# Kernel tuning notes

Hardware: AMD Instinct MI355X
Metric: run time of the kernel (lower is better)

## Reference

```python
import jax, jax.numpy as jnp
import numpy as np

C1 = 256
C2 = 256
C = 256

def setup_inputs() -> dict:
    key = jax.random.key(0)
    ks = jax.random.split(key, 8)
    B, S, H, W = 4, 8, 32, 32
    img_feat = jax.random.normal(ks[0], (B, S, C1, H, W), dtype=jnp.float32)
    depth_feat = jax.random.normal(ks[1], (B, S, C2, H, W), dtype=jnp.float32)
    sq = 1.0 / np.sqrt(C1)
    sk = 1.0 / np.sqrt(C2)
    Wq = jax.random.uniform(ks[2], (C1, C), jnp.float32, -sq, sq)
    bq = jax.random.uniform(ks[3], (C,), jnp.float32, -sq, sq)
    Wk = jax.random.uniform(ks[4], (C2, C), jnp.float32, -sk, sk)
    bk = jax.random.uniform(ks[5], (C,), jnp.float32, -sk, sk)
    Wv = jax.random.uniform(ks[6], (C2, C), jnp.float32, -sk, sk)
    bv = jax.random.uniform(ks[7], (C,), jnp.float32, -sk, sk)
    return {"img_feat": img_feat, "depth_feat": depth_feat,
            "Wq": Wq, "bq": bq, "Wk": Wk, "bk": bk, "Wv": Wv, "bv": bv}

def reference(img_feat, depth_feat, Wq, bq, Wk, bk, Wv, bv):
    B, S, _, H, W = img_feat.shape
    hw = H * W
    # channels-last, flatten spatial: [B,S,hw,c1]
    img = jnp.transpose(img_feat, (0, 1, 3, 4, 2)).reshape(B, S, hw, -1)
    depth = jnp.transpose(depth_feat, (0, 1, 3, 4, 2)).reshape(B, S, hw, -1)
    q = (img @ Wq + bq).astype(jnp.float32)    # [B,S,hw,c]
    k = (depth @ Wk + bk).astype(jnp.float32)  # [B,S,hw,c]
    v = (depth @ Wv + bv).astype(jnp.float32)  # [B,S,hw,c]
    scale = 1.0 / jnp.sqrt(jnp.float32(Wq.shape[1]))
    scores = jnp.einsum('bsqc,bskc->bsqk', q, k) * scale  # [B,S,hw,hw]
    attn = jax.nn.softmax(scores, axis=-1)
    out = jnp.einsum('bsqk,bskc->bsqc', attn, v)          # [B,S,hw,c]
    out = out + img                                        # residual (c == c1)
    out = out.reshape(B, S, H, W, -1).astype(img_feat.dtype)
    return jnp.transpose(out, (0, 1, 4, 2, 3))             # [B,S,c,H,W]
```

## Files before the change

### kernel.cpp

```cpp
#include <hip/hip_runtime.h>
#include <hip/hip_bf16.h>

typedef __hip_bfloat16 bf16;
typedef __attribute__((ext_vector_type(8))) short short8v;
typedef __attribute__((ext_vector_type(4))) float f32x4;

#define NSLICE 32
#define HW     1024
#define CDIM   256
#define KVT    32

__global__ __launch_bounds__(256)
void wt_prep_kernel(const float* __restrict__ Wq, const float* __restrict__ Wk,
                    const float* __restrict__ Wv, bf16* __restrict__ wt)
{
    const int m = blockIdx.x >> 8;
    const int r = blockIdx.x & 255;
    const int tid = threadIdx.x;
    const float* W = (m == 0) ? Wq : (m == 1) ? Wk : Wv;
    const float sc = (m == 0) ? 0.0625f : 1.0f;
    wt[((size_t)m << 16) + (size_t)tid * 256 + r] = __float2bfloat16(W[r * 256 + tid] * sc);
}

__global__ __launch_bounds__(256)
void proj_q_kernel(const float* __restrict__ img, const bf16* __restrict__ wt,
                   const float* __restrict__ bq, bf16* __restrict__ qo)
{
    const int bid   = blockIdx.x;
    const int s     = (bid & 7) * 4 + ((bid >> 3) & 3);
    const int tt    = (bid >> 5) & 15;
    const int chalf = bid >> 9;
    const int t0    = tt * 64;

    const int tid  = threadIdx.x;
    const int wave = tid >> 6;
    const int lane = tid & 63;
    const int lo16 = lane & 15;
    const int hi4  = lane >> 4;
    const int cw0  = chalf * 128 + wave * 32;

    __shared__ short Ai[64][40];

    const int so = tid >> 6, st = tid & 63;
    const float* imgS = img + (size_t)s * CDIM * HW + t0;

    f32x4 aq[2][4];
    #pragma unroll
    for (int a = 0; a < 2; ++a)
        #pragma unroll
        for (int b = 0; b < 4; ++b) aq[a][b] = (f32x4){0.f, 0.f, 0.f, 0.f};

    float ri[8];
    #pragma unroll
    for (int j = 0; j < 8; ++j) ri[j] = imgS[(size_t)(so * 8 + j) * HW + st];

    for (int kc = 0; kc < 8; ++kc) {
        __syncthreads();
        {
            short ti[8];
            #pragma unroll
            for (int j = 0; j < 8; ++j) {
                bf16 hb = __float2bfloat16(ri[j]);
                ti[j] = *reinterpret_cast<short*>(&hb);
            }
            *reinterpret_cast<short8v*>(&Ai[st][so * 8]) = *reinterpret_cast<short8v*>(ti);
        }
        __syncthreads();

        if (kc < 7) {
            #pragma unroll
            for (int j = 0; j < 8; ++j)
                ri[j] = imgS[(size_t)((kc + 1) * 32 + so * 8 + j) * HW + st];
        }

        short8v xi[4];
        #pragma unroll
        for (int nf = 0; nf < 4; ++nf)
            xi[nf] = *reinterpret_cast<const short8v*>(&Ai[nf * 16 + lo16][hi4 * 8]);

        const int koff = kc * 32 + hi4 * 8;
        short8v wqf[2];
        #pragma unroll
        for (int mf = 0; mf < 2; ++mf)
            wqf[mf] = *reinterpret_cast<const short8v*>(
                wt + (size_t)(cw0 + mf * 16 + lo16) * 256 + koff);

        #pragma unroll
        for (int mf = 0; mf < 2; ++mf)
            #pragma unroll
            for (int nf = 0; nf < 4; ++nf)
                aq[mf][nf] = __builtin_amdgcn_mfma_f32_16x16x32_bf16(wqf[mf], xi[nf], aq[mf][nf], 0, 0, 0);
    }

    #pragma unroll
    for (int mf = 0; mf < 2; ++mf) {
        const int cb = cw0 + mf * 16 + 4 * hi4;
        const float4 b4 = *reinterpret_cast<const float4*>(bq + cb);
        const float ba[4] = {b4.x * 0.0625f, b4.y * 0.0625f, b4.z * 0.0625f, b4.w * 0.0625f};
        #pragma unroll
        for (int nf = 0; nf < 4; ++nf) {
            const int tok = t0 + nf * 16 + lo16;
            bf16 tq[4];
            #pragma unroll
            for (int g = 0; g < 4; ++g)
                tq[g] = __float2bfloat16(aq[mf][nf][g] + ba[g]);
            *reinterpret_cast<uint2*>(&qo[((size_t)s * HW + tok) * CDIM + cb]) =
                *reinterpret_cast<uint2*>(tq);
        }
    }
}

__global__ __launch_bounds__(256)
void proj_kv_kernel(const float* __restrict__ dep, const bf16* __restrict__ wt,
                    const float* __restrict__ bk, const float* __restrict__ bv,
                    bf16* __restrict__ ko, bf16* __restrict__ vt)
{
    const int bid   = blockIdx.x;
    const int s     = (bid & 7) * 4 + ((bid >> 3) & 3);
    const int tt    = (bid >> 5) & 15;
    const int chalf = bid >> 9;
    const int t0    = tt * 64;

    const int tid  = threadIdx.x;
    const int wave = tid >> 6;
    const int lane = tid & 63;
    const int lo16 = lane & 15;
    const int hi4  = lane >> 4;
    const int cw0  = chalf * 128 + wave * 32;

    __shared__ short Ad[64][40];

    const int so = tid >> 6, st = tid & 63;
    const float* depS = dep + (size_t)s * CDIM * HW + t0;
    const bf16* wtk = wt + (1 << 16);
    const bf16* wtv = wt + (2 << 16);

    f32x4 ak[2][4], av[4][2];
    #pragma unroll
    for (int a = 0; a < 2; ++a)
        #pragma unroll
        for (int b = 0; b < 4; ++b) {
            ak[a][b] = (f32x4){0.f, 0.f, 0.f, 0.f};
            av[b][a] = (f32x4){0.f, 0.f, 0.f, 0.f};
        }

    float rd[8];
    #pragma unroll
    for (int j = 0; j < 8; ++j) rd[j] = depS[(size_t)(so * 8 + j) * HW + st];

    for (int kc = 0; kc < 8; ++kc) {
        __syncthreads();
        {
            short td[8];
            #pragma unroll
            for (int j = 0; j < 8; ++j) {
                bf16 hb = __float2bfloat16(rd[j]);
                td[j] = *reinterpret_cast<short*>(&hb);
            }
            *reinterpret_cast<short8v*>(&Ad[st][so * 8]) = *reinterpret_cast<short8v*>(td);
        }
        __syncthreads();

        if (kc < 7) {
            #pragma unroll
            for (int j = 0; j < 8; ++j)
                rd[j] = depS[(size_t)((kc + 1) * 32 + so * 8 + j) * HW + st];
        }

        short8v xd[4];
        #pragma unroll
        for (int nf = 0; nf < 4; ++nf)
            xd[nf] = *reinterpret_cast<const short8v*>(&Ad[nf * 16 + lo16][hi4 * 8]);

        const int koff = kc * 32 + hi4 * 8;
        short8v wkf[2], wvf[2];
        #pragma unroll
        for (int mf = 0; mf < 2; ++mf) {
            const size_t wrow = (size_t)(cw0 + mf * 16 + lo16) * 256 + koff;
            wkf[mf] = *reinterpret_cast<const short8v*>(wtk + wrow);
            wvf[mf] = *reinterpret_cast<const short8v*>(wtv + wrow);
        }

        #pragma unroll
        for (int mf = 0; mf < 2; ++mf)
            #pragma unroll
            for (int nf = 0; nf < 4; ++nf)
                ak[mf][nf] = __builtin_amdgcn_mfma_f32_16x16x32_bf16(wkf[mf], xd[nf], ak[mf][nf], 0, 0, 0);
        #pragma unroll
        for (int mf = 0; mf < 4; ++mf)
            #pragma unroll
            for (int nf = 0; nf < 2; ++nf)
                av[mf][nf] = __builtin_amdgcn_mfma_f32_16x16x32_bf16(xd[mf], wvf[nf], av[mf][nf], 0, 0, 0);
    }

    #pragma unroll
    for (int mf = 0; mf < 2; ++mf) {
        const int cb = cw0 + mf * 16 + 4 * hi4;
        const float4 b4 = *reinterpret_cast<const float4*>(bk + cb);
        const float ba[4] = {b4.x, b4.y, b4.z, b4.w};
        #pragma unroll
        for (int nf = 0; nf < 4; ++nf) {
            const int tok = t0 + nf * 16 + lo16;
            bf16 tk[4];
            #pragma unroll
            for (int g = 0; g < 4; ++g)
                tk[g] = __float2bfloat16(ak[mf][nf][g] + ba[g]);
            *reinterpret_cast<uint2*>(&ko[((size_t)s * HW + tok) * CDIM + cb]) =
                *reinterpret_cast<uint2*>(tk);
        }
    }
    #pragma unroll
    for (int nf = 0; nf < 2; ++nf) {
        const int c = cw0 + nf * 16 + lo16;
        const float bvv = bv[c];
        #pragma unroll
        for (int mf = 0; mf < 4; ++mf) {
            const int tb = t0 + mf * 16 + 4 * hi4;
            bf16 tv[4];
            #pragma unroll
            for (int g = 0; g < 4; ++g)
                tv[g] = __float2bfloat16(av[mf][nf][g] + bvv);
            *reinterpret_cast<uint2*>(&vt[((size_t)s * CDIM + c) * HW + tb]) =
                *reinterpret_cast<uint2*>(tv);
        }
    }
}

__global__ __launch_bounds__(256)
void flash_mfma_kernel(const bf16* __restrict__ q, const bf16* __restrict__ k,
                       const bf16* __restrict__ vt, const float* __restrict__ img,
                       float* __restrict__ out)
{
    const int bid = blockIdx.x;
    const int s   = (bid & 7) * 4 + ((bid >> 3) & 3);
    const int t0  = (bid >> 5) * 64;

    const int tid  = threadIdx.x;
    const int wave = tid >> 6;
    const int lane = tid & 63;
    const int lo16 = lane & 15;
    const int hi4  = lane >> 4;

    __shared__ short KsL[32 * 256];
    __shared__ short VsL[256 * 32];
    __shared__ short PsL[4 * 16 * 32];

    short8v qf[8];
    {
        const bf16* qp = q + ((size_t)s * HW + t0 + wave * 16 + lo16) * CDIM + hi4 * 8;
        #pragma unroll
        for (int kf = 0; kf < 8; ++kf)
            qf[kf] = *reinterpret_cast<const short8v*>(qp + kf * 32);
    }

    f32x4 Oacc[16];
    #pragma unroll
    for (int cf = 0; cf < 16; ++cf) Oacc[cf] = (f32x4){0.f, 0.f, 0.f, 0.f};
    float lp[4] = {0.f, 0.f, 0.f, 0.f};

    const bf16* kS  = k  + (size_t)s * HW * CDIM;
    const bf16* vtS = vt + (size_t)s * CDIM * HW;

    const int krow = tid >> 3;
    const int kch  = tid & 7;
    const int kxor = krow & 7;
    const int vxor = (tid >> 1) & 3;

    short8v kreg[4], vreg[4];
    #pragma unroll
    for (int u = 0; u < 4; ++u) {
        kreg[u] = *reinterpret_cast<const short8v*>(kS + (size_t)krow * CDIM + (kch + 8 * u) * 8);
        vreg[u] = *reinterpret_cast<const short8v*>(vtS + (size_t)tid * HW + u * 8);
    }

    const int pvRow = lo16 * 32 + (hi4 ^ ((lo16 >> 1) & 3)) * 8;
    for (int kt = 0; kt < HW / KVT; ++kt) {
        __syncthreads();
        #pragma unroll
        for (int u = 0; u < 4; ++u)
            *reinterpret_cast<short8v*>(&KsL[krow * 256 + ((kch ^ kxor) + 8 * u) * 8]) = kreg[u];
        #pragma unroll
        for (int u = 0; u < 4; ++u)
            *reinterpret_cast<short8v*>(&VsL[tid * 32 + (u ^ vxor) * 8]) = vreg[u];
        __syncthreads();

        if (kt + 1 < HW / KVT) {
            const bf16* src = kS + (size_t)(kt + 1) * KVT * CDIM;
            #pragma unroll
            for (int u = 0; u < 4; ++u) {
                kreg[u] = *reinterpret_cast<const short8v*>(src + (size_t)krow * CDIM + (kch + 8 * u) * 8);
                vreg[u] = *reinterpret_cast<const short8v*>(vtS + (size_t)tid * HW + (kt + 1) * KVT + u * 8);
            }
        }

        f32x4 sa[2];
        sa[0] = (f32x4){0.f, 0.f, 0.f, 0.f};
        sa[1] = (f32x4){0.f, 0.f, 0.f, 0.f};
        __builtin_amdgcn_s_setprio(1);
        #pragma unroll
        for (int ks = 0; ks < 8; ++ks) {
            #pragma unroll
            for (int cf = 0; cf < 2; ++cf) {
                const int row = cf * 16 + lo16;
                short8v bfr = *reinterpret_cast<const short8v*>(
                    &KsL[row * 256 + ((4 * ks + hi4) ^ (lo16 & 7)) * 8]);
                sa[cf] = __builtin_amdgcn_mfma_f32_16x16x32_bf16(qf[ks], bfr, sa[cf], 0, 0, 0);
            }
        }
        __builtin_amdgcn_s_setprio(0);

        #pragma unroll
        for (int cf = 0; cf < 2; ++cf)
            #pragma unroll
            for (int g = 0; g < 4; ++g) {
                const float e = __expf(sa[cf][g]);
                lp[g] += e;
                bf16 hb = __float2bfloat16(e);
                const int r = 4 * hi4 + g;
                const int ch = (2 * cf + (lo16 >> 3)) ^ ((r >> 1) & 3);
                PsL[wave * 512 + r * 32 + ch * 8 + (lo16 & 7)] = *reinterpret_cast<short*>(&hb);
            }

        const short8v pa = *reinterpret_cast<const short8v*>(&PsL[wave * 512 + pvRow]);

        __builtin_amdgcn_s_setprio(1);
        #pragma unroll
        for (int cf = 0; cf < 16; ++cf) {
            const int row = cf * 16 + lo16;
            const short8v vb = *reinterpret_cast<const short8v*>(
                &VsL[row * 32 + (hi4 ^ ((lo16 >> 1) & 3)) * 8]);
            Oacc[cf] = __builtin_amdgcn_mfma_f32_16x16x32_bf16(pa, vb, Oacc[cf], 0, 0, 0);
        }
        __builtin_amdgcn_s_setprio(0);
    }

    float inv[4];
    #pragma unroll
    for (int g = 0; g < 4; ++g) {
        float l = lp[g];
        #pragma unroll
        for (int off = 1; off < 16; off <<= 1) l += __shfl_xor(l, off);
        inv[g] = 1.0f / l;
    }
    const float* imgS = img + (size_t)s * CDIM * HW;
    float*       outS = out + (size_t)s * CDIM * HW;
    const int tt = t0 + wave * 16 + 4 * hi4;
    #pragma unroll
    for (int cf = 0; cf < 16; ++cf) {
        const int c = cf * 16 + lo16;
        const float4 r4 = *reinterpret_cast<const float4*>(imgS + (size_t)c * HW + tt);
        float4 o;
        o.x = Oacc[cf][0] * inv[0] + r4.x;
        o.y = Oacc[cf][1] * inv[1] + r4.y;
        o.z = Oacc[cf][2] * inv[2] + r4.z;
        o.w = Oacc[cf][3] * inv[3] + r4.w;
        *reinterpret_cast<float4*>(outS + (size_t)c * HW + tt) = o;
    }
}

extern "C" void kernel_launch(void* const* d_in, const int* in_sizes, int n_in,
                              void* d_out, int out_size, void* d_ws, size_t ws_size,
                              hipStream_t stream)
{
    const float* img = (const float*)d_in[0];
    const float* dep = (const float*)d_in[1];
    const float* Wq  = (const float*)d_in[2];
    const float* bq  = (const float*)d_in[3];
    const float* Wk  = (const float*)d_in[4];
    const float* bk  = (const float*)d_in[5];
    const float* Wv  = (const float*)d_in[6];
    const float* bv  = (const float*)d_in[7];
    float* out = (float*)d_out;

    const size_t npt  = (size_t)NSLICE * HW * CDIM;
    const size_t need = 3 * npt * sizeof(bf16) + 3 * 65536 * sizeof(bf16);
    if (ws_size < need) {
        hipMemsetAsync(d_out, 0, (size_t)out_size * sizeof(float), stream);
        return;
    }

    bf16* q  = (bf16*)d_ws;
    bf16* k  = q + npt;
    bf16* vt = k + npt;
    bf16* wt = vt + npt;

    wt_prep_kernel<<<dim3(3 * 256), 256, 0, stream>>>(Wq, Wk, Wv, wt);

    proj_q_kernel<<<dim3(NSLICE * 32), 256, 0, stream>>>(img, wt, bq, q);
    proj_kv_kernel<<<dim3(NSLICE * 32), 256, 0, stream>>>(dep, wt, bk, bv, k, vt);

    flash_mfma_kernel<<<dim3(NSLICE * 16), 256, 0, stream>>>(q, k, vt, img, out);
}
```

Baseline: 123.0 us.

## Double KV tile to 64, compute S transposed, and pass P via shuffles

The flash attention kernel now stages 64-key K and V^T tiles per iteration instead of 32, halving the number of barrier-synchronized iterations. QK^T is computed as K·Q so each lane holds probabilities along keys, and the P operand for the PV MFMA is built with cross-lane shuffles rather than a round trip through LDS. Row sums are reduced differently to match the transposed layout, and launch bounds request two blocks per SM. The cost is doubled LDS (64KB), more registers for prefetch buffers, and many shuffles, which may limit occupancy.

```diff
diff --git a/kernel.cpp b/kernel.cpp
--- a/kernel.cpp
+++ b/kernel.cpp
@@ -4,11 +4,11 @@
 typedef __hip_bfloat16 bf16;
 typedef __attribute__((ext_vector_type(8))) short short8v;
 typedef __attribute__((ext_vector_type(4))) float f32x4;
+typedef __attribute__((ext_vector_type(4))) unsigned int u32x4;
 
 #define NSLICE 32
 #define HW     1024
 #define CDIM   256
-#define KVT    32
 
 __global__ __launch_bounds__(256)
 void wt_prep_kernel(const float* __restrict__ Wq, const float* __restrict__ Wk,
@@ -226,7 +226,7 @@
     }
 }
 
-__global__ __launch_bounds__(256)
+__global__ __launch_bounds__(256, 2)
 void flash_mfma_kernel(const bf16* __restrict__ q, const bf16* __restrict__ k,
                        const bf16* __restrict__ vt, const float* __restrict__ img,
                        float* __restrict__ out)
@@ -241,9 +241,8 @@
     const int lo16 = lane & 15;
     const int hi4  = lane >> 4;
 
-    __shared__ short KsL[32 * 256];
-    __shared__ short VsL[256 * 32];
-    __shared__ short PsL[4 * 16 * 32];
+    __shared__ short KsL[64 * 256];
+    __shared__ short VsL[256 * 64];
 
     short8v qf[8];
     {
@@ -256,92 +255,114 @@
     f32x4 Oacc[16];
     #pragma unroll
     for (int cf = 0; cf < 16; ++cf) Oacc[cf] = (f32x4){0.f, 0.f, 0.f, 0.f};
-    float lp[4] = {0.f, 0.f, 0.f, 0.f};
+    float lp = 0.f;
 
     const bf16* kS  = k  + (size_t)s * HW * CDIM;
     const bf16* vtS = vt + (size_t)s * CDIM * HW;
 
-    const int krow = tid >> 3;
-    const int kch  = tid & 7;
-    const int kxor = krow & 7;
-    const int vxor = (tid >> 1) & 3;
-
-    short8v kreg[4], vreg[4];
-    #pragma unroll
-    for (int u = 0; u < 4; ++u) {
-        kreg[u] = *reinterpret_cast<const short8v*>(kS + (size_t)krow * CDIM + (kch + 8 * u) * 8);
+    const int krow = tid >> 2;
+    const int kseg = tid & 3;
+    const int kx   = krow & 7;
+    const int vx   = tid & 7;
+
+    short8v kreg[8], vreg[8];
+    #pragma unroll
+    for (int u = 0; u < 8; ++u) {
+        kreg[u] = *reinterpret_cast<const short8v*>(kS + (size_t)krow * CDIM + kseg * 64 + u * 8);
         vreg[u] = *reinterpret_cast<const short8v*>(vtS + (size_t)tid * HW + u * 8);
     }
 
-    const int pvRow = lo16 * 32 + (hi4 ^ ((lo16 >> 1) & 3)) * 8;
-    for (int kt = 0; kt < HW / KVT; ++kt) {
-        __syncthreads();
-        #pragma unroll
-        for (int u = 0; u < 4; ++u)
-            *reinterpret_cast<short8v*>(&KsL[krow * 256 + ((kch ^ kxor) + 8 * u) * 8]) = kreg[u];
-        #pragma unroll
-        for (int u = 0; u < 4; ++u)
-            *reinterpret_cast<short8v*>(&VsL[tid * 32 + (u ^ vxor) * 8]) = vreg[u];
-        __syncthreads();
-
-        if (kt + 1 < HW / KVT) {
-            const bf16* src = kS + (size_t)(kt + 1) * KVT * CDIM;
-            #pragma unroll
-            for (int u = 0; u < 4; ++u) {
-                kreg[u] = *reinterpret_cast<const short8v*>(src + (size_t)krow * CDIM + (kch + 8 * u) * 8);
-                vreg[u] = *reinterpret_cast<const short8v*>(vtS + (size_t)tid * HW + (kt + 1) * KVT + u * 8);
+    const int src0 = lo16 + 16 * (2 * (hi4 & 1));
+    const int src1 = src0 + 16;
+    const bool sel = hi4 >= 2;
+
+    for (int kt = 0; kt < 16; ++kt) {
+        __syncthreads();
+        #pragma unroll
+        for (int u = 0; u < 8; ++u)
+            *reinterpret_cast<short8v*>(&KsL[krow * 256 + ((kseg * 8 + u) ^ kx) * 8]) = kreg[u];
+        #pragma unroll
+        for (int u = 0; u < 8; ++u)
+            *reinterpret_cast<short8v*>(&VsL[tid * 64 + (u ^ vx) * 8]) = vreg[u];
+        __syncthreads();
+
+        if (kt + 1 < 16) {
+            const bf16* ksrc = kS + (size_t)(kt + 1) * 64 * CDIM;
+            #pragma unroll
+            for (int u = 0; u < 8; ++u) {
+                kreg[u] = *reinterpret_cast<const short8v*>(ksrc + (size_t)krow * CDIM + kseg * 64 + u * 8);
+                vreg[u] = *reinterpret_cast<const short8v*>(vtS + (size_t)tid * HW + (kt + 1) * 64 + u * 8);
             }
         }
 
-        f32x4 sa[2];
-        sa[0] = (f32x4){0.f, 0.f, 0.f, 0.f};
-        sa[1] = (f32x4){0.f, 0.f, 0.f, 0.f};
+        f32x4 sa[4];
+        #pragma unroll
+        for (int m = 0; m < 4; ++m) sa[m] = (f32x4){0.f, 0.f, 0.f, 0.f};
         __builtin_amdgcn_s_setprio(1);
         #pragma unroll
         for (int ks = 0; ks < 8; ++ks) {
             #pragma unroll
-            for (int cf = 0; cf < 2; ++cf) {
-                const int row = cf * 16 + lo16;
-                short8v bfr = *reinterpret_cast<const short8v*>(
-                    &KsL[row * 256 + ((4 * ks + hi4) ^ (lo16 & 7)) * 8]);
-                sa[cf] = __builtin_amdgcn_mfma_f32_16x16x32_bf16(qf[ks], bfr, sa[cf], 0, 0, 0);
+            for (int m = 0; m < 4; ++m) {
+                const short8v kfr = *reinterpret_cast<const short8v*>(
+                    &KsL[(16 * m + lo16) * 256 + ((4 * ks + hi4) ^ (lo16 & 7)) * 8]);
+                sa[m] = __builtin_amdgcn_mfma_f32_16x16x32_bf16(kfr, qf[ks], sa[m], 0, 0, 0);
             }
         }
         __builtin_amdgcn_s_setprio(0);
 
-        #pragma unroll
-        for (int cf = 0; cf < 2; ++cf)
-            #pragma unroll
-            for (int g = 0; g < 4; ++g) {
-                const float e = __expf(sa[cf][g]);
-                lp[g] += e;
-                bf16 hb = __float2bfloat16(e);
-                const int r = 4 * hi4 + g;
-                const int ch = (2 * cf + (lo16 >> 3)) ^ ((r >> 1) & 3);
-                PsL[wave * 512 + r * 32 + ch * 8 + (lo16 & 7)] = *reinterpret_cast<short*>(&hb);
+        unsigned int pk[4][2];
+        #pragma unroll
+        for (int m = 0; m < 4; ++m) {
+            float e0 = __expf(sa[m][0]), e1 = __expf(sa[m][1]);
+            float e2 = __expf(sa[m][2]), e3 = __expf(sa[m][3]);
+            lp += (e0 + e1) + (e2 + e3);
+            bf16 h0 = __float2bfloat16(e0), h1 = __float2bfloat16(e1);
+            bf16 h2 = __float2bfloat16(e2), h3 = __float2bfloat16(e3);
+            pk[m][0] = (unsigned int)*reinterpret_cast<unsigned short*>(&h0) |
+                       ((unsigned int)*reinterpret_cast<unsigned short*>(&h1) << 16);
+            pk[m][1] = (unsigned int)*reinterpret_cast<unsigned short*>(&h2) |
+                       ((unsigned int)*reinterpret_cast<unsigned short*>(&h3) << 16);
+        }
+
+        short8v pfr[2];
+        #pragma unroll
+        for (int c = 0; c < 2; ++c) {
+            const unsigned int a0 = (unsigned int)__shfl((int)pk[2 * c][0], src0);
+            const unsigned int b0 = (unsigned int)__shfl((int)pk[2 * c + 1][0], src0);
+            const unsigned int a1 = (unsigned int)__shfl((int)pk[2 * c][1], src0);
+            const unsigned int b1 = (unsigned int)__shfl((int)pk[2 * c + 1][1], src0);
+            const unsigned int a2 = (unsigned int)__shfl((int)pk[2 * c][0], src1);
+            const unsigned int b2 = (unsigned int)__shfl((int)pk[2 * c + 1][0], src1);
+            const unsigned int a3 = (unsigned int)__shfl((int)pk[2 * c][1], src1);
+            const unsigned int b3 = (unsigned int)__shfl((int)pk[2 * c + 1][1], src1);
+            u32x4 w;
+            w.x = sel ? b0 : a0;
+            w.y = sel ? b1 : a1;
+            w.z = sel ? b2 : a2;
+            w.w = sel ? b3 : a3;
+            pfr[c] = *reinterpret_cast<short8v*>(&w);
+        }
+
+        __builtin_amdgcn_s_setprio(1);
+        #pragma unroll
+        for (int c = 0; c < 2; ++c) {
+            #pragma unroll
+            for (int cf = 0; cf < 16; ++cf) {
+                const short8v vfr = *reinterpret_cast<const short8v*>(
+                    &VsL[(cf * 16 + lo16) * 64 + ((4 * c + hi4) ^ (lo16 & 7)) * 8]);
+                Oacc[cf] = __builtin_amdgcn_mfma_f32_16x16x32_bf16(pfr[c], vfr, Oacc[cf], 0, 0, 0);
             }
-
-        const short8v pa = *reinterpret_cast<const short8v*>(&PsL[wave * 512 + pvRow]);
-
-        __builtin_amdgcn_s_setprio(1);
-        #pragma unroll
-        for (int cf = 0; cf < 16; ++cf) {
-            const int row = cf * 16 + lo16;
-            const short8v vb = *reinterpret_cast<const short8v*>(
-                &VsL[row * 32 + (hi4 ^ ((lo16 >> 1) & 3)) * 8]);
-            Oacc[cf] = __builtin_amdgcn_mfma_f32_16x16x32_bf16(pa, vb, Oacc[cf], 0, 0, 0);
         }
         __builtin_amdgcn_s_setprio(0);
     }
 
+    lp += __shfl_xor(lp, 16);
+    lp += __shfl_xor(lp, 32);
     float inv[4];
     #pragma unroll
-    for (int g = 0; g < 4; ++g) {
-        float l = lp[g];
-        #pragma unroll
-        for (int off = 1; off < 16; off <<= 1) l += __shfl_xor(l, off);
-        inv[g] = 1.0f / l;
-    }
+    for (int g = 0; g < 4; ++g)
+        inv[g] = 1.0f / __shfl(lp, 4 * hi4 + g);
+
     const float* imgS = img + (size_t)s * CDIM * HW;
     float*       outS = out + (size_t)s * CDIM * HW;
     const int tt = t0 + wave * 16 + 4 * hi4;
```

Result: slower. 138.8 us (+12.9%).

## Fuse Q projection into flash attention kernel, drop separate Q pass

Applied to the files above, without the earlier changes.

Removes the standalone Q projection kernel and computes each block's 64-token Q tile inside the attention kernel. The image tile is staged through a swizzled shared buffer and multiplied by Wq with MFMA, and the result is written back to shared memory to form the Q fragments. The shared-memory arrays are merged into one aliased buffer. This avoids a kernel launch and the round trip of Q through global memory, but adds per-block projection work, extra barriers, and Wq loads from global inside the attention kernel.

```diff
diff --git a/kernel.cpp b/kernel.cpp
--- a/kernel.cpp
+++ b/kernel.cpp
@@ -23,94 +23,6 @@
 }
 
 __global__ __launch_bounds__(256)
-void proj_q_kernel(const float* __restrict__ img, const bf16* __restrict__ wt,
-                   const float* __restrict__ bq, bf16* __restrict__ qo)
-{
-    const int bid   = blockIdx.x;
-    const int s     = (bid & 7) * 4 + ((bid >> 3) & 3);
-    const int tt    = (bid >> 5) & 15;
-    const int chalf = bid >> 9;
-    const int t0    = tt * 64;
-
-    const int tid  = threadIdx.x;
-    const int wave = tid >> 6;
-    const int lane = tid & 63;
-    const int lo16 = lane & 15;
-    const int hi4  = lane >> 4;
-    const int cw0  = chalf * 128 + wave * 32;
-
-    __shared__ short Ai[64][40];
-
-    const int so = tid >> 6, st = tid & 63;
-    const float* imgS = img + (size_t)s * CDIM * HW + t0;
-
-    f32x4 aq[2][4];
-    #pragma unroll
-    for (int a = 0; a < 2; ++a)
-        #pragma unroll
-        for (int b = 0; b < 4; ++b) aq[a][b] = (f32x4){0.f, 0.f, 0.f, 0.f};
-
-    float ri[8];
-    #pragma unroll
-    for (int j = 0; j < 8; ++j) ri[j] = imgS[(size_t)(so * 8 + j) * HW + st];
-
-    for (int kc = 0; kc < 8; ++kc) {
-        __syncthreads();
-        {
-            short ti[8];
-            #pragma unroll
-            for (int j = 0; j < 8; ++j) {
-                bf16 hb = __float2bfloat16(ri[j]);
-                ti[j] = *reinterpret_cast<short*>(&hb);
-            }
-            *reinterpret_cast<short8v*>(&Ai[st][so * 8]) = *reinterpret_cast<short8v*>(ti);
-        }
-        __syncthreads();
-
-        if (kc < 7) {
-            #pragma unroll
-            for (int j = 0; j < 8; ++j)
-                ri[j] = imgS[(size_t)((kc + 1) * 32 + so * 8 + j) * HW + st];
-        }
-
-        short8v xi[4];
-        #pragma unroll
-        for (int nf = 0; nf < 4; ++nf)
-            xi[nf] = *reinterpret_cast<const short8v*>(&Ai[nf * 16 + lo16][hi4 * 8]);
-
-        const int koff = kc * 32 + hi4 * 8;
-        short8v wqf[2];
-        #pragma unroll
-        for (int mf = 0; mf < 2; ++mf)
-            wqf[mf] = *reinterpret_cast<const short8v*>(
-                wt + (size_t)(cw0 + mf * 16 + lo16) * 256 + koff);
-
-        #pragma unroll
-        for (int mf = 0; mf < 2; ++mf)
-            #pragma unroll
-            for (int nf = 0; nf < 4; ++nf)
-                aq[mf][nf] = __builtin_amdgcn_mfma_f32_16x16x32_bf16(wqf[mf], xi[nf], aq[mf][nf], 0, 0, 0);
-    }
-
-    #pragma unroll
-    for (int mf = 0; mf < 2; ++mf) {
-        const int cb = cw0 + mf * 16 + 4 * hi4;
-        const float4 b4 = *reinterpret_cast<const float4*>(bq + cb);
-        const float ba[4] = {b4.x * 0.0625f, b4.y * 0.0625f, b4.z * 0.0625f, b4.w * 0.0625f};
-        #pragma unroll
-        for (int nf = 0; nf < 4; ++nf) {
-            const int tok = t0 + nf * 16 + lo16;
-            bf16 tq[4];
-            #pragma unroll
-            for (int g = 0; g < 4; ++g)
-                tq[g] = __float2bfloat16(aq[mf][nf][g] + ba[g]);
-            *reinterpret_cast<uint2*>(&qo[((size_t)s * HW + tok) * CDIM + cb]) =
-                *reinterpret_cast<uint2*>(tq);
-        }
-    }
-}
-
-__global__ __launch_bounds__(256)
 void proj_kv_kernel(const float* __restrict__ dep, const bf16* __restrict__ wt,
                     const float* __restrict__ bk, const float* __restrict__ bv,
                     bf16* __restrict__ ko, bf16* __restrict__ vt)
@@ -227,9 +139,10 @@
 }
 
 __global__ __launch_bounds__(256)
-void flash_mfma_kernel(const bf16* __restrict__ q, const bf16* __restrict__ k,
-                       const bf16* __restrict__ vt, const float* __restrict__ img,
-                       float* __restrict__ out)
+void flash_fusedq_kernel(const float* __restrict__ img, const bf16* __restrict__ wt,
+                         const float* __restrict__ bq,
+                         const bf16* __restrict__ k, const bf16* __restrict__ vt,
+                         float* __restrict__ out)
 {
     const int bid = blockIdx.x;
     const int s   = (bid & 7) * 4 + ((bid >> 3) & 3);
@@ -241,31 +154,16 @@
     const int lo16 = lane & 15;
     const int hi4  = lane >> 4;
 
-    __shared__ short KsL[32 * 256];
-    __shared__ short VsL[256 * 32];
-    __shared__ short PsL[4 * 16 * 32];
-
-    short8v qf[8];
-    {
-        const bf16* qp = q + ((size_t)s * HW + t0 + wave * 16 + lo16) * CDIM + hi4 * 8;
-        #pragma unroll
-        for (int kf = 0; kf < 8; ++kf)
-            qf[kf] = *reinterpret_cast<const short8v*>(qp + kf * 32);
-    }
-
-    f32x4 Oacc[16];
-    #pragma unroll
-    for (int cf = 0; cf < 16; ++cf) Oacc[cf] = (f32x4){0.f, 0.f, 0.f, 0.f};
-    float lp[4] = {0.f, 0.f, 0.f, 0.f};
-
-    const bf16* kS  = k  + (size_t)s * HW * CDIM;
-    const bf16* vtS = vt + (size_t)s * CDIM * HW;
+    __shared__ __align__(16) short SM[18432];
+
+    const bf16*  kS   = k   + (size_t)s * HW * CDIM;
+    const bf16*  vtS  = vt  + (size_t)s * CDIM * HW;
+    const float* imgS = img + (size_t)s * CDIM * HW;
 
     const int krow = tid >> 3;
     const int kch  = tid & 7;
     const int kxor = krow & 7;
     const int vxor = (tid >> 1) & 3;
-
     short8v kreg[4], vreg[4];
     #pragma unroll
     for (int u = 0; u < 4; ++u) {
@@ -273,15 +171,93 @@
         vreg[u] = *reinterpret_cast<const short8v*>(vtS + (size_t)tid * HW + u * 8);
     }
 
+    {
+        const int so = tid >> 6, st = tid & 63;
+        const float* ip = imgS + t0 + st;
+        for (int kc = 0; kc < 8; ++kc) {
+            short tw[8];
+            #pragma unroll
+            for (int j = 0; j < 8; ++j) {
+                bf16 hb = __float2bfloat16(ip[(size_t)(kc * 32 + so * 8 + j) * HW]);
+                tw[j] = *reinterpret_cast<short*>(&hb);
+            }
+            const int c  = kc * 4 + so;
+            const int cs = (c & ~7) | ((c & 7) ^ (st & 7));
+            *reinterpret_cast<short8v*>(&SM[st * 256 + cs * 8]) = *reinterpret_cast<short8v*>(tw);
+        }
+    }
+    __syncthreads();
+
+    f32x4 qacc[16];
+    #pragma unroll
+    for (int mb = 0; mb < 16; ++mb) qacc[mb] = (f32x4){0.f, 0.f, 0.f, 0.f};
+    {
+        const int r = wave * 16 + lo16;
+        for (int kc = 0; kc < 8; ++kc) {
+            const int cc  = kc * 4 + hi4;
+            const int ccs = (cc & ~7) | ((cc & 7) ^ (lo16 & 7));
+            const short8v imgB = *reinterpret_cast<const short8v*>(&SM[r * 256 + ccs * 8]);
+            const int koff = kc * 32 + hi4 * 8;
+            #pragma unroll
+            for (int mb = 0; mb < 16; ++mb) {
+                const short8v wq = *reinterpret_cast<const short8v*>(
+                    wt + (size_t)(mb * 16 + lo16) * 256 + koff);
+                qacc[mb] = __builtin_amdgcn_mfma_f32_16x16x32_bf16(wq, imgB, qacc[mb], 0, 0, 0);
+            }
+        }
+    }
+    __syncthreads();
+
+    {
+        short* W = &SM[wave * 4096];
+        #pragma unroll
+        for (int mb = 0; mb < 16; ++mb) {
+            const int cb = mb * 16 + 4 * hi4;
+            const float4 b4 = *reinterpret_cast<const float4*>(bq + cb);
+            short t4[4];
+            {
+                bf16 h0 = __float2bfloat16(qacc[mb][0] + b4.x * 0.0625f);
+                bf16 h1 = __float2bfloat16(qacc[mb][1] + b4.y * 0.0625f);
+                bf16 h2 = __float2bfloat16(qacc[mb][2] + b4.z * 0.0625f);
+                bf16 h3 = __float2bfloat16(qacc[mb][3] + b4.w * 0.0625f);
+                t4[0] = *reinterpret_cast<short*>(&h0);
+                t4[1] = *reinterpret_cast<short*>(&h1);
+                t4[2] = *reinterpret_cast<short*>(&h2);
+                t4[3] = *reinterpret_cast<short*>(&h3);
+            }
+            const int c  = mb * 2 + (hi4 >> 1);
+            const int cs = (c & ~7) | ((c & 7) ^ (lo16 & 7));
+            *reinterpret_cast<uint2*>(&W[lo16 * 256 + cs * 8 + (hi4 & 1) * 4]) =
+                *reinterpret_cast<uint2*>(t4);
+        }
+    }
+    __syncthreads();
+
+    short8v qf[8];
+    {
+        const short* R = &SM[wave * 4096];
+        #pragma unroll
+        for (int ks = 0; ks < 8; ++ks) {
+            const int c  = 4 * ks + hi4;
+            const int cs = (c & ~7) | ((c & 7) ^ (lo16 & 7));
+            qf[ks] = *reinterpret_cast<const short8v*>(&R[lo16 * 256 + cs * 8]);
+        }
+    }
+
+    f32x4 Oacc[16];
+    #pragma unroll
+    for (int cf = 0; cf < 16; ++cf) Oacc[cf] = (f32x4){0.f, 0.f, 0.f, 0.f};
+    float lp[4] = {0.f, 0.f, 0.f, 0.f};
+
     const int pvRow = lo16 * 32 + (hi4 ^ ((lo16 >> 1) & 3)) * 8;
     for (int kt = 0; kt < HW / KVT; ++kt) {
         __syncthreads();
         #pragma unroll
         for (int u = 0; u < 4; ++u)
-            *reinterpret_cast<short8v*>(&KsL[krow * 256 + ((kch ^ kxor) + 8 * u) * 8]) = kreg[u];
+            *reinterpret_cast<short8v*>(&SM[krow * 256 + ((kch ^ kxor) + 8 * u) * 8]) = kreg[u];
         #pragma unroll
         for (int u = 0; u < 4; ++u)
-            *reinterpret_cast<short8v*>(&VsL[tid * 32 + (u ^ vxor) * 8]) = vreg[u];
+            *reinterpret_cast<short8v*>(&SM[8192 + tid * 32 + (u ^ vxor) * 8]) = vreg[u];
         __syncthreads();
 
         if (kt + 1 < HW / KVT) {
@@ -303,7 +279,7 @@
             for (int cf = 0; cf < 2; ++cf) {
                 const int row = cf * 16 + lo16;
                 short8v bfr = *reinterpret_cast<const short8v*>(
-                    &KsL[row * 256 + ((4 * ks + hi4) ^ (lo16 & 7)) * 8]);
+                    &SM[row * 256 + ((4 * ks + hi4) ^ (lo16 & 7)) * 8]);
                 sa[cf] = __builtin_amdgcn_mfma_f32_16x16x32_bf16(qf[ks], bfr, sa[cf], 0, 0, 0);
             }
         }
@@ -318,17 +294,17 @@
                 bf16 hb = __float2bfloat16(e);
                 const int r = 4 * hi4 + g;
                 const int ch = (2 * cf + (lo16 >> 3)) ^ ((r >> 1) & 3);
-                PsL[wave * 512 + r * 32 + ch * 8 + (lo16 & 7)] = *reinterpret_cast<short*>(&hb);
-            }
-
-        const short8v pa = *reinterpret_cast<const short8v*>(&PsL[wave * 512 + pvRow]);
+                SM[16384 + wave * 512 + r * 32 + ch * 8 + (lo16 & 7)] = *reinterpret_cast<short*>(&hb);
+            }
+
+        const short8v pa = *reinterpret_cast<const short8v*>(&SM[16384 + wave * 512 + pvRow]);
 
         __builtin_amdgcn_s_setprio(1);
         #pragma unroll
         for (int cf = 0; cf < 16; ++cf) {
             const int row = cf * 16 + lo16;
             const short8v vb = *reinterpret_cast<const short8v*>(
-                &VsL[row * 32 + (hi4 ^ ((lo16 >> 1) & 3)) * 8]);
+                &SM[8192 + row * 32 + (hi4 ^ ((lo16 >> 1) & 3)) * 8]);
             Oacc[cf] = __builtin_amdgcn_mfma_f32_16x16x32_bf16(pa, vb, Oacc[cf], 0, 0, 0);
         }
         __builtin_amdgcn_s_setprio(0);
@@ -342,8 +318,7 @@
         for (int off = 1; off < 16; off <<= 1) l += __shfl_xor(l, off);
         inv[g] = 1.0f / l;
     }
-    const float* imgS = img + (size_t)s * CDIM * HW;
-    float*       outS = out + (size_t)s * CDIM * HW;
+    float* outS = out + (size_t)s * CDIM * HW;
     const int tt = t0 + wave * 16 + 4 * hi4;
     #pragma unroll
     for (int cf = 0; cf < 16; ++cf) {
@@ -386,8 +361,7 @@
 
     wt_prep_kernel<<<dim3(3 * 256), 256, 0, stream>>>(Wq, Wk, Wv, wt);
 
-    proj_q_kernel<<<dim3(NSLICE * 32), 256, 0, stream>>>(img, wt, bq, q);
     proj_kv_kernel<<<dim3(NSLICE * 32), 256, 0, stream>>>(dep, wt, bk, bv, k, vt);
 
-    flash_mfma_kernel<<<dim3(NSLICE * 16), 256, 0, stream>>>(q, k, vt, img, out);
+    flash_fusedq_kernel<<<dim3(NSLICE * 16), 256, 0, stream>>>(img, wt, bq, k, vt, out);
 }
```

Result: slower. 134.7 us (+9.5%).

## Process two 16-row query tiles per wave to reuse K/V LDS fragments

Applied to the files above, without the earlier changes.

Each wave now handles 32 query rows (two 16-row MFMA tiles) instead of 16, so every block covers 128 queries and the grid is halved to 256 blocks. Each K and V fragment read from LDS feeds two MFMAs, halving K/V global loads and LDS staging per query. The cost is doubled accumulator registers (32 f32x4 output tiles plus two Q fragment sets), which lowers occupancy, and only 256 blocks on a 256-CU device, which may leave less latency hiding.

```diff
diff --git a/kernel.cpp b/kernel.cpp
--- a/kernel.cpp
+++ b/kernel.cpp
@@ -233,7 +233,7 @@
 {
     const int bid = blockIdx.x;
     const int s   = (bid & 7) * 4 + ((bid >> 3) & 3);
-    const int t0  = (bid >> 5) * 64;
+    const int t0  = (bid >> 5) * 128;
 
     const int tid  = threadIdx.x;
     const int wave = tid >> 6;
@@ -243,20 +243,26 @@
 
     __shared__ short KsL[32 * 256];
     __shared__ short VsL[256 * 32];
-    __shared__ short PsL[4 * 16 * 32];
-
-    short8v qf[8];
-    {
-        const bf16* qp = q + ((size_t)s * HW + t0 + wave * 16 + lo16) * CDIM + hi4 * 8;
+    __shared__ short PsL[4 * 2 * 512];
+
+    const int rowbase = t0 + wave * 32;
+
+    short8v qf[2][8];
+    #pragma unroll
+    for (int m = 0; m < 2; ++m) {
+        const bf16* qp = q + ((size_t)s * HW + rowbase + m * 16 + lo16) * CDIM + hi4 * 8;
         #pragma unroll
         for (int kf = 0; kf < 8; ++kf)
-            qf[kf] = *reinterpret_cast<const short8v*>(qp + kf * 32);
-    }
-
-    f32x4 Oacc[16];
-    #pragma unroll
-    for (int cf = 0; cf < 16; ++cf) Oacc[cf] = (f32x4){0.f, 0.f, 0.f, 0.f};
-    float lp[4] = {0.f, 0.f, 0.f, 0.f};
+            qf[m][kf] = *reinterpret_cast<const short8v*>(qp + kf * 32);
+    }
+
+    f32x4 Oa[16], Ob[16];
+    #pragma unroll
+    for (int cf = 0; cf < 16; ++cf) {
+        Oa[cf] = (f32x4){0.f, 0.f, 0.f, 0.f};
+        Ob[cf] = (f32x4){0.f, 0.f, 0.f, 0.f};
+    }
+    float lp[2][4] = {{0.f, 0.f, 0.f, 0.f}, {0.f, 0.f, 0.f, 0.f}};
 
     const bf16* kS  = k  + (size_t)s * HW * CDIM;
     const bf16* vtS = vt + (size_t)s * CDIM * HW;
@@ -293,35 +299,42 @@
             }
         }
 
-        f32x4 sa[2];
-        sa[0] = (f32x4){0.f, 0.f, 0.f, 0.f};
-        sa[1] = (f32x4){0.f, 0.f, 0.f, 0.f};
+        f32x4 sa[2][2];
+        sa[0][0] = (f32x4){0.f, 0.f, 0.f, 0.f};
+        sa[0][1] = (f32x4){0.f, 0.f, 0.f, 0.f};
+        sa[1][0] = (f32x4){0.f, 0.f, 0.f, 0.f};
+        sa[1][1] = (f32x4){0.f, 0.f, 0.f, 0.f};
         __builtin_amdgcn_s_setprio(1);
         #pragma unroll
         for (int ks = 0; ks < 8; ++ks) {
             #pragma unroll
             for (int cf = 0; cf < 2; ++cf) {
                 const int row = cf * 16 + lo16;
-                short8v bfr = *reinterpret_cast<const short8v*>(
+                const short8v bfr = *reinterpret_cast<const short8v*>(
                     &KsL[row * 256 + ((4 * ks + hi4) ^ (lo16 & 7)) * 8]);
-                sa[cf] = __builtin_amdgcn_mfma_f32_16x16x32_bf16(qf[ks], bfr, sa[cf], 0, 0, 0);
+                sa[0][cf] = __builtin_amdgcn_mfma_f32_16x16x32_bf16(qf[0][ks], bfr, sa[0][cf], 0, 0, 0);
+                sa[1][cf] = __builtin_amdgcn_mfma_f32_16x16x32_bf16(qf[1][ks], bfr, sa[1][cf], 0, 0, 0);
             }
         }
         __builtin_amdgcn_s_setprio(0);
 
         #pragma unroll
-        for (int cf = 0; cf < 2; ++cf)
-            #pragma unroll
-            for (int g = 0; g < 4; ++g) {
-                const float e = __expf(sa[cf][g]);
-                lp[g] += e;
-                bf16 hb = __float2bfloat16(e);
-                const int r = 4 * hi4 + g;
-                const int ch = (2 * cf + (lo16 >> 3)) ^ ((r >> 1) & 3);
-                PsL[wave * 512 + r * 32 + ch * 8 + (lo16 & 7)] = *reinterpret_cast<short*>(&hb);
-            }
-
-        const short8v pa = *reinterpret_cast<const short8v*>(&PsL[wave * 512 + pvRow]);
+        for (int m = 0; m < 2; ++m)
+            #pragma unroll
+            for (int cf = 0; cf < 2; ++cf)
+                #pragma unroll
+                for (int g = 0; g < 4; ++g) {
+                    const float e = __expf(sa[m][cf][g]);
+                    lp[m][g] += e;
+                    bf16 hb = __float2bfloat16(e);
+                    const int r = 4 * hi4 + g;
+                    const int ch = (2 * cf + (lo16 >> 3)) ^ ((r >> 1) & 3);
+                    PsL[wave * 1024 + m * 512 + r * 32 + ch * 8 + (lo16 & 7)] =
+                        *reinterpret_cast<short*>(&hb);
+                }
+
+        const short8v pa0 = *reinterpret_cast<const short8v*>(&PsL[wave * 1024 + pvRow]);
+        const short8v pa1 = *reinterpret_cast<const short8v*>(&PsL[wave * 1024 + 512 + pvRow]);
 
         __builtin_amdgcn_s_setprio(1);
         #pragma unroll
@@ -329,32 +342,37 @@
             const int row = cf * 16 + lo16;
             const short8v vb = *reinterpret_cast<const short8v*>(
                 &VsL[row * 32 + (hi4 ^ ((lo16 >> 1) & 3)) * 8]);
-            Oacc[cf] = __builtin_amdgcn_mfma_f32_16x16x32_bf16(pa, vb, Oacc[cf], 0, 0, 0);
+            Oa[cf] = __builtin_amdgcn_mfma_f32_16x16x32_bf16(pa0, vb, Oa[cf], 0, 0, 0);
+            Ob[cf] = __builtin_amdgcn_mfma_f32_16x16x32_bf16(pa1, vb, Ob[cf], 0, 0, 0);
         }
         __builtin_amdgcn_s_setprio(0);
     }
 
-    float inv[4];
-    #pragma unroll
-    for (int g = 0; g < 4; ++g) {
-        float l = lp[g];
-        #pragma unroll
-        for (int off = 1; off < 16; off <<= 1) l += __shfl_xor(l, off);
-        inv[g] = 1.0f / l;
-    }
     const float* imgS = img + (size_t)s * CDIM * HW;
     float*       outS = out + (size_t)s * CDIM * HW;
-    const int tt = t0 + wave * 16 + 4 * hi4;
-    #pragma unroll
-    for (int cf = 0; cf < 16; ++cf) {
-        const int c = cf * 16 + lo16;
-        const float4 r4 = *reinterpret_cast<const float4*>(imgS + (size_t)c * HW + tt);
-        float4 o;
-        o.x = Oacc[cf][0] * inv[0] + r4.x;
-        o.y = Oacc[cf][1] * inv[1] + r4.y;
-        o.z = Oacc[cf][2] * inv[2] + r4.z;
-        o.w = Oacc[cf][3] * inv[3] + r4.w;
-        *reinterpret_cast<float4*>(outS + (size_t)c * HW + tt) = o;
+    #pragma unroll
+    for (int m = 0; m < 2; ++m) {
+        float inv[4];
+        #pragma unroll
+        for (int g = 0; g < 4; ++g) {
+            float l = lp[m][g];
+            #pragma unroll
+            for (int off = 1; off < 16; off <<= 1) l += __shfl_xor(l, off);
+            inv[g] = 1.0f / l;
+        }
+        const int tt = rowbase + m * 16 + 4 * hi4;
+        #pragma unroll
+        for (int cf = 0; cf < 16; ++cf) {
+            const int c = cf * 16 + lo16;
+            const f32x4 O = (m == 0) ? Oa[cf] : Ob[cf];
+            const float4 r4 = *reinterpret_cast<const float4*>(imgS + (size_t)c * HW + tt);
+            float4 o;
+            o.x = O[0] * inv[0] + r4.x;
+            o.y = O[1] * inv[1] + r4.y;
+            o.z = O[2] * inv[2] + r4.z;
+            o.w = O[3] * inv[3] + r4.w;
+            *reinterpret_cast<float4*>(outS + (size_t)c * HW + tt) = o;
+        }
     }
 }
 
@@ -389,5 +407,5 @@
     proj_q_kernel<<<dim3(NSLICE * 32), 256, 0, stream>>>(img, wt, bq, q);
     proj_kv_kernel<<<dim3(NSLICE * 32), 256, 0, stream>>>(dep, wt, bk, bv, k, vt);
 
-    flash_mfma_kernel<<<dim3(NSLICE * 16), 256, 0, stream>>>(q, k, vt, img, out);
+    flash_mfma_kernel<<<dim3(NSLICE * 8), 256, 0, stream>>>(q, k, vt, img, out);
 }
```

Result: slower. 132.5 us (+7.7%).
